# Kernel tuning notes

Measured on AMD Instinct MI355X. Metric: run time of the kernel, lower is better.

The kernel has to match this reference:

```python
import jax, jax.numpy as jnp
import numpy as np

N_NODES = 100000
N_EDGES = 1600000
D_IN = 64
D_H = 64


def setup_inputs() -> dict:
    key = jax.random.key(0)
    ks = jax.random.split(key, 8)
    inp = {
        "in_feat": jax.random.normal(ks[0], (N_NODES, D_IN), dtype=jnp.float32),
        "src": jax.random.randint(ks[1], (N_EDGES,), 0, N_NODES, dtype=jnp.int64)
        if jax.config.jax_enable_x64
        else jax.random.randint(ks[1], (N_EDGES,), 0, N_NODES).astype(jnp.int32),
        "dst": jax.random.randint(ks[2], (N_EDGES,), 0, N_NODES).astype(jnp.int32),
        "W_self1": jax.random.normal(ks[3], (D_H, D_IN), dtype=jnp.float32) * 0.1,
        "W_neigh1": jax.random.normal(ks[4], (D_H, D_IN), dtype=jnp.float32) * 0.1,
        "b1": jnp.zeros((D_H,), dtype=jnp.float32),
        "W_self2": jax.random.normal(ks[5], (D_H, D_H), dtype=jnp.float32) * 0.1,
        "W_neigh2": jax.random.normal(ks[6], (D_H, D_H), dtype=jnp.float32) * 0.1,
        "b2": jnp.zeros((D_H,), dtype=jnp.float32),
    }
    inp["src"] = inp["src"].astype(jnp.int32)
    return inp


def _sage_mean(x, src, dst, W_self, W_neigh, b, n_nodes):
    # mean aggregation over incoming edges: gather src feats, segment-sum at dst
    msg_sum = jax.ops.segment_sum(x[src], dst, num_segments=n_nodes)  # [N, D]
    deg = jax.ops.segment_sum(jnp.ones_like(dst, dtype=x.dtype), dst, num_segments=n_nodes)
    h_neigh = msg_sum / jnp.maximum(deg, 1.0)[:, None]
    # DGL SAGEConv: fc_self(h) + fc_neigh(h_neigh) + bias
    return x @ W_self.T + h_neigh @ W_neigh.T + b


def reference(in_feat, src, dst, W_self1, W_neigh1, b1, W_self2, W_neigh2, b2):
    n = in_feat.shape[0]
    h = _sage_mean(in_feat, src, dst, W_self1, W_neigh1, b1, n)
    # dropout in eval mode is identity; then relu
    h = jax.nn.relu(h)
    h = _sage_mean(h, src, dst, W_self2, W_neigh2, b2, n)
    return h
```

## Files before the change

### kernel.cpp

```cpp
#include <hip/hip_runtime.h>

#define NN 100000
#define NE 1600000
#define NROWS 100032
#define CAP 48
#define ZOFF (NN * 64)
#define NRANGE 12500
#define SCAT_GROUPS 8
#define SCAT_CHUNKS 196
#define SCAT_EPB 8192
#define SCAT_BLKS (SCAT_GROUPS * SCAT_CHUNKS)
#define CAST_BLKS 6250
#define WCAT_BLKS 64
#define ZCUR_BLKS 391
#define AGG_BLKS 3125

typedef __attribute__((ext_vector_type(8))) short short8;
typedef __attribute__((ext_vector_type(4))) float float4v;
typedef __attribute__((ext_vector_type(4))) int int4v;

__device__ inline unsigned short f2bf(float f)
{
    union { float f; unsigned u; } v; v.f = f;
    unsigned r = v.u + 0x7FFF + ((v.u >> 16) & 1);
    return (unsigned short)(r >> 16);
}
__device__ inline float bf2f(unsigned short h)
{
    union { unsigned u; float f; } v; v.u = ((unsigned)h) << 16; return v.f;
}

__global__ __launch_bounds__(256) void zero_kernel(int* __restrict__ cur)
{
    int i = blockIdx.x * 256 + threadIdx.x;
    if (i < NN) cur[i] = 0;
}

__global__ __launch_bounds__(256) void prep_kernel(
    const float* __restrict__ x,
    const float* __restrict__ Ws1, const float* __restrict__ Wn1,
    const float* __restrict__ Ws2, const float* __restrict__ Wn2,
    const int* __restrict__ src, const int* __restrict__ dst,
    unsigned short* __restrict__ XF, unsigned short* __restrict__ H1,
    unsigned short* __restrict__ W1, unsigned short* __restrict__ W2,
    int* __restrict__ cur, int* __restrict__ colb)
{
    const int b = blockIdx.x;
    const int tid = threadIdx.x;
    if (b < SCAT_BLKS) {
        const int g = b & 7;
        const int chunk = b >> 3;
        const int lo = g * NRANGE;
        const int hi = lo + NRANGE;
        const int base = chunk * SCAT_EPB;
        #pragma unroll
        for (int k = 0; k < 8; ++k) {
            int e = base + (k * 256 + tid) * 4;
            if (e < NE) {
                int4v s4 = __builtin_nontemporal_load((const int4v*)(src + e));
                int4v d4 = __builtin_nontemporal_load((const int4v*)(dst + e));
                int p;
                if (d4[0] >= lo && d4[0] < hi) {
                    p = atomicAdd(&cur[d4[0]], 1);
                    if (p < CAP) colb[(size_t)d4[0] * CAP + p] = s4[0] << 6;
                }
                if (d4[1] >= lo && d4[1] < hi) {
                    p = atomicAdd(&cur[d4[1]], 1);
                    if (p < CAP) colb[(size_t)d4[1] * CAP + p] = s4[1] << 6;
                }
                if (d4[2] >= lo && d4[2] < hi) {
                    p = atomicAdd(&cur[d4[2]], 1);
                    if (p < CAP) colb[(size_t)d4[2] * CAP + p] = s4[2] << 6;
                }
                if (d4[3] >= lo && d4[3] < hi) {
                    p = atomicAdd(&cur[d4[3]], 1);
                    if (p < CAP) colb[(size_t)d4[3] * CAP + p] = s4[3] << 6;
                }
            }
        }
    } else if (b < SCAT_BLKS + CAST_BLKS) {
        int t = (b - SCAT_BLKS) * 256 + tid;
        int n = t >> 4;
        int k4 = (t & 15) * 4;
        float4v v = __builtin_nontemporal_load(
            (const float4v*)(x + (size_t)n * 64 + k4));
        ushort4 o;
        o.x = f2bf(v[0]); o.y = f2bf(v[1]); o.z = f2bf(v[2]); o.w = f2bf(v[3]);
        *(ushort4*)(XF + (size_t)n * 64 + k4) = o;
    } else if (b < SCAT_BLKS + CAST_BLKS + WCAT_BLKS) {
        int id = (b - SCAT_BLKS - CAST_BLKS) * 256 + tid;
        int l = id >> 13;
        int r = id & 8191;
        int o = r >> 7, k = r & 127;
        const float* Ws = l ? Ws2 : Ws1;
        const float* Wn = l ? Wn2 : Wn1;
        float v = (k < 64) ? Ws[o * 64 + k] : Wn[o * 64 + (k - 64)];
        (l ? W2 : W1)[r] = f2bf(v);
    } else {
        if (tid < 32) {
            ushort4 z; z.x = 0; z.y = 0; z.z = 0; z.w = 0;
            unsigned short* base = (tid < 16) ? XF : H1;
            *(ushort4*)(base + (size_t)NN * 64 + (tid & 15) * 4) = z;
        }
    }
}

template <int LAYER1>
__global__ __launch_bounds__(256) void aggdense_kernel(
    const unsigned short* __restrict__ XIN,
    const int* __restrict__ cur,
    const int* __restrict__ colb,
    const unsigned short* __restrict__ Wcat,
    const float* __restrict__ bias,
    unsigned short* __restrict__ xout,
    float* __restrict__ fout)
{
    __shared__ __align__(16) unsigned short HN[32 * 72];
    const int tid = threadIdx.x;
    const int wave = tid >> 6;
    const int lane = tid & 63;
    const int g = lane >> 4;
    const int q = lane & 15;
    const int nbase = blockIdx.x * 32 + wave * 8;

    int cntv = (lane < 8) ? cur[nbase + lane] : 0;

    int cnt_nx = __shfl(cntv, 0, 64);
    int cc_nx = min(cnt_nx, CAP);
    int ci_nx = (lane < cc_nx) ? colb[(size_t)nbase * CAP + lane] : ZOFF;

    for (int i = 0; i < 8; ++i) {
        int n = nbase + i;
        int cnt = cnt_nx, cc = cc_nx, ci = ci_nx;
        if (i < 7) {
            cnt_nx = __shfl(cntv, i + 1, 64);
            cc_nx = min(cnt_nx, CAP);
            ci_nx = (lane < cc_nx) ? colb[(size_t)(n + 1) * CAP + lane] : ZOFF;
        }
        float a0 = 0.f, a1 = 0.f, a2 = 0.f, a3 = 0.f;
        for (int t = 0; t < cc; t += 16) {
            int i0 = __shfl(ci, t + g, 64);
            int i1 = __shfl(ci, t + 4 + g, 64);
            int i2 = __shfl(ci, t + 8 + g, 64);
            int i3 = __shfl(ci, t + 12 + g, 64);
            ushort4 v0 = *(const ushort4*)(XIN + i0 + q * 4);
            ushort4 v1 = *(const ushort4*)(XIN + i1 + q * 4);
            ushort4 v2 = *(const ushort4*)(XIN + i2 + q * 4);
            ushort4 v3 = *(const ushort4*)(XIN + i3 + q * 4);
            a0 += bf2f(v0.x) + bf2f(v1.x) + bf2f(v2.x) + bf2f(v3.x);
            a1 += bf2f(v0.y) + bf2f(v1.y) + bf2f(v2.y) + bf2f(v3.y);
            a2 += bf2f(v0.z) + bf2f(v1.z) + bf2f(v2.z) + bf2f(v3.z);
            a3 += bf2f(v0.w) + bf2f(v1.w) + bf2f(v2.w) + bf2f(v3.w);
        }
        a0 += __shfl_xor(a0, 16, 64); a0 += __shfl_xor(a0, 32, 64);
        a1 += __shfl_xor(a1, 16, 64); a1 += __shfl_xor(a1, 32, 64);
        a2 += __shfl_xor(a2, 16, 64); a2 += __shfl_xor(a2, 32, 64);
        a3 += __shfl_xor(a3, 16, 64); a3 += __shfl_xor(a3, 32, 64);
        float rdeg = 1.0f / fmaxf((float)cnt, 1.0f);
        if (g == 0) {
            ushort4 o;
            o.x = f2bf(a0 * rdeg); o.y = f2bf(a1 * rdeg);
            o.z = f2bf(a2 * rdeg); o.w = f2bf(a3 * rdeg);
            *(ushort4*)(&HN[(wave * 8 + i) * 72 + q * 4]) = o;
        }
    }
    __syncthreads();

    if (wave < 2) {
        const int mrow = lane & 15;
        const int kb = lane >> 4;
        const int row0 = blockIdx.x * 32 + wave * 16;

        short8 a[4];
        {
            const short* ax = (const short*)XIN + (size_t)(row0 + mrow) * 64 + kb * 8;
            const short* ah = (const short*)HN + (wave * 16 + mrow) * 72 + kb * 8;
            a[0] = *(const short8*)(ax);
            a[1] = *(const short8*)(ax + 32);
            a[2] = *(const short8*)(ah);
            a[3] = *(const short8*)(ah + 32);
        }

        float4v acc[4];
        #pragma unroll
        for (int c = 0; c < 4; ++c) acc[c] = (float4v){0.f, 0.f, 0.f, 0.f};

        #pragma unroll
        for (int c = 0; c < 4; ++c) {
            const short* brow = (const short*)Wcat + (c * 16 + mrow) * 128 + kb * 8;
            #pragma unroll
            for (int i = 0; i < 4; ++i) {
                short8 bfr = *(const short8*)(brow + i * 32);
                acc[c] = __builtin_amdgcn_mfma_f32_16x16x32_bf16(a[i], bfr, acc[c], 0, 0, 0);
            }
        }

        const int rbase = row0 + kb * 4;
        #pragma unroll
        for (int c = 0; c < 4; ++c) {
            int o = c * 16 + mrow;
            float bv = bias[o];
            #pragma unroll
            for (int r = 0; r < 4; ++r) {
                int node = rbase + r;
                float val = acc[c][r] + bv;
                if (LAYER1) {
                    xout[(size_t)node * 64 + o] = f2bf(fmaxf(val, 0.f));
                } else {
                    fout[(size_t)node * 64 + o] = val;
                }
            }
        }
    }
}

extern "C" void kernel_launch(void* const* d_in, const int* in_sizes, int n_in,
                              void* d_out, int out_size, void* d_ws, size_t ws_size,
                              hipStream_t stream)
{
    const float* in_feat = (const float*)d_in[0];
    const int*   src     = (const int*)d_in[1];
    const int*   dst     = (const int*)d_in[2];
    const float* Ws1     = (const float*)d_in[3];
    const float* Wn1     = (const float*)d_in[4];
    const float* b1      = (const float*)d_in[5];
    const float* Ws2     = (const float*)d_in[6];
    const float* Wn2     = (const float*)d_in[7];
    const float* b2      = (const float*)d_in[8];
    float* out = (float*)d_out;

    int* cur  = (int*)d_ws;
    int* colb = cur + NN;
    unsigned short* XF = (unsigned short*)(colb + (size_t)NN * CAP);
    unsigned short* H1 = XF + (size_t)NROWS * 64;
    unsigned short* W1 = H1 + (size_t)NROWS * 64;
    unsigned short* W2 = W1 + 8192;

    zero_kernel<<<ZCUR_BLKS, 256, 0, stream>>>(cur);

    prep_kernel<<<SCAT_BLKS + CAST_BLKS + WCAT_BLKS + 1, 256, 0, stream>>>(
        in_feat, Ws1, Wn1, Ws2, Wn2, src, dst, XF, H1, W1, W2, cur, colb);

    aggdense_kernel<1><<<AGG_BLKS, 256, 0, stream>>>(
        XF, cur, colb, W1, b1, H1, nullptr);

    aggdense_kernel<0><<<AGG_BLKS, 256, 0, stream>>>(
        H1, cur, colb, W2, b2, nullptr, out);
}
```

Baseline: 251.7 us.

## Split aggregation and dense into separate kernels with feature-sliced layout

Stores node features in four 16-column slices so each aggregation block gathers only a 32-byte slice per neighbor, which improves cache locality of the random gathers. The fused agg+dense kernel is split into a separate aggregation kernel (one node per 8 lanes, one slice per block) and a dense MFMA kernel that uses all four waves. Layer-1 output overwrites the input buffer in place. The cost is two extra kernel launches and a write and re-read of the aggregated features through global memory.

```diff
diff --git a/kernel.cpp b/kernel.cpp
--- a/kernel.cpp
+++ b/kernel.cpp
@@ -3,8 +3,9 @@
 #define NN 100000
 #define NE 1600000
 #define NROWS 100032
+#define SROW NROWS
 #define CAP 48
-#define ZOFF (NN * 64)
+#define DUMMY NN
 #define NRANGE 12500
 #define SCAT_GROUPS 8
 #define SCAT_CHUNKS 196
@@ -13,7 +14,9 @@
 #define CAST_BLKS 6250
 #define WCAT_BLKS 64
 #define ZCUR_BLKS 391
-#define AGG_BLKS 3125
+#define PAD_BLKS 2
+#define AGG_BLKS 12504
+#define DENSE_BLKS 1563
 
 typedef __attribute__((ext_vector_type(8))) short short8;
 typedef __attribute__((ext_vector_type(4))) float float4v;
@@ -41,7 +44,7 @@
     const float* __restrict__ Ws1, const float* __restrict__ Wn1,
     const float* __restrict__ Ws2, const float* __restrict__ Wn2,
     const int* __restrict__ src, const int* __restrict__ dst,
-    unsigned short* __restrict__ XF, unsigned short* __restrict__ H1,
+    unsigned short* __restrict__ XS, unsigned short* __restrict__ HNs,
     unsigned short* __restrict__ W1, unsigned short* __restrict__ W2,
     int* __restrict__ cur, int* __restrict__ colb)
 {
@@ -62,19 +65,19 @@
                 int p;
                 if (d4[0] >= lo && d4[0] < hi) {
                     p = atomicAdd(&cur[d4[0]], 1);
-                    if (p < CAP) colb[(size_t)d4[0] * CAP + p] = s4[0] << 6;
+                    if (p < CAP) colb[(size_t)d4[0] * CAP + p] = s4[0];
                 }
                 if (d4[1] >= lo && d4[1] < hi) {
                     p = atomicAdd(&cur[d4[1]], 1);
-                    if (p < CAP) colb[(size_t)d4[1] * CAP + p] = s4[1] << 6;
+                    if (p < CAP) colb[(size_t)d4[1] * CAP + p] = s4[1];
                 }
                 if (d4[2] >= lo && d4[2] < hi) {
                     p = atomicAdd(&cur[d4[2]], 1);
-                    if (p < CAP) colb[(size_t)d4[2] * CAP + p] = s4[2] << 6;
+                    if (p < CAP) colb[(size_t)d4[2] * CAP + p] = s4[2];
                 }
                 if (d4[3] >= lo && d4[3] < hi) {
                     p = atomicAdd(&cur[d4[3]], 1);
-                    if (p < CAP) colb[(size_t)d4[3] * CAP + p] = s4[3] << 6;
+                    if (p < CAP) colb[(size_t)d4[3] * CAP + p] = s4[3];
                 }
             }
         }
@@ -86,7 +89,7 @@
             (const float4v*)(x + (size_t)n * 64 + k4));
         ushort4 o;
         o.x = f2bf(v[0]); o.y = f2bf(v[1]); o.z = f2bf(v[2]); o.w = f2bf(v[3]);
-        *(ushort4*)(XF + (size_t)n * 64 + k4) = o;
+        *(ushort4*)(XS + ((size_t)(k4 >> 4) * SROW + n) * 16 + (k4 & 15)) = o;
     } else if (b < SCAT_BLKS + CAST_BLKS + WCAT_BLKS) {
         int id = (b - SCAT_BLKS - CAST_BLKS) * 256 + tid;
         int l = id >> 13;
@@ -97,118 +100,149 @@
         float v = (k < 64) ? Ws[o * 64 + k] : Wn[o * 64 + (k - 64)];
         (l ? W2 : W1)[r] = f2bf(v);
     } else {
-        if (tid < 32) {
+        unsigned short* base = (b == SCAT_BLKS + CAST_BLKS + WCAT_BLKS) ? XS : HNs;
+        for (int i = tid; i < 512; i += 256) {
+            int f = i >> 7;
+            int r = (i >> 2) & 31;
+            int q = i & 3;
             ushort4 z; z.x = 0; z.y = 0; z.z = 0; z.w = 0;
-            unsigned short* base = (tid < 16) ? XF : H1;
-            *(ushort4*)(base + (size_t)NN * 64 + (tid & 15) * 4) = z;
-        }
-    }
-}
-
-template <int LAYER1>
-__global__ __launch_bounds__(256) void aggdense_kernel(
-    const unsigned short* __restrict__ XIN,
+            *(ushort4*)(base + ((size_t)f * SROW + NN + r) * 16 + q * 4) = z;
+        }
+    }
+}
+
+__global__ __launch_bounds__(256) void agg_kernel(
+    const unsigned short* __restrict__ XS,
     const int* __restrict__ cur,
     const int* __restrict__ colb,
-    const unsigned short* __restrict__ Wcat,
-    const float* __restrict__ bias,
-    unsigned short* __restrict__ xout,
-    float* __restrict__ fout)
-{
-    __shared__ __align__(16) unsigned short HN[32 * 72];
+    unsigned short* __restrict__ HNs)
+{
+    const int b = blockIdx.x;
+    const int f = (b & 7) >> 1;
+    const int chunk = ((b >> 3) << 1) | (b & 1);
+    if (chunk >= NN / 32) return;
     const int tid = threadIdx.x;
     const int wave = tid >> 6;
     const int lane = tid & 63;
-    const int g = lane >> 4;
-    const int q = lane & 15;
-    const int nbase = blockIdx.x * 32 + wave * 8;
-
-    int cntv = (lane < 8) ? cur[nbase + lane] : 0;
-
-    int cnt_nx = __shfl(cntv, 0, 64);
-    int cc_nx = min(cnt_nx, CAP);
-    int ci_nx = (lane < cc_nx) ? colb[(size_t)nbase * CAP + lane] : ZOFF;
-
-    for (int i = 0; i < 8; ++i) {
-        int n = nbase + i;
-        int cnt = cnt_nx, cc = cc_nx, ci = ci_nx;
-        if (i < 7) {
-            cnt_nx = __shfl(cntv, i + 1, 64);
-            cc_nx = min(cnt_nx, CAP);
-            ci_nx = (lane < cc_nx) ? colb[(size_t)(n + 1) * CAP + lane] : ZOFF;
-        }
-        float a0 = 0.f, a1 = 0.f, a2 = 0.f, a3 = 0.f;
-        for (int t = 0; t < cc; t += 16) {
-            int i0 = __shfl(ci, t + g, 64);
-            int i1 = __shfl(ci, t + 4 + g, 64);
-            int i2 = __shfl(ci, t + 8 + g, 64);
-            int i3 = __shfl(ci, t + 12 + g, 64);
-            ushort4 v0 = *(const ushort4*)(XIN + i0 + q * 4);
-            ushort4 v1 = *(const ushort4*)(XIN + i1 + q * 4);
-            ushort4 v2 = *(const ushort4*)(XIN + i2 + q * 4);
-            ushort4 v3 = *(const ushort4*)(XIN + i3 + q * 4);
-            a0 += bf2f(v0.x) + bf2f(v1.x) + bf2f(v2.x) + bf2f(v3.x);
-            a1 += bf2f(v0.y) + bf2f(v1.y) + bf2f(v2.y) + bf2f(v3.y);
-            a2 += bf2f(v0.z) + bf2f(v1.z) + bf2f(v2.z) + bf2f(v3.z);
-            a3 += bf2f(v0.w) + bf2f(v1.w) + bf2f(v2.w) + bf2f(v3.w);
-        }
-        a0 += __shfl_xor(a0, 16, 64); a0 += __shfl_xor(a0, 32, 64);
-        a1 += __shfl_xor(a1, 16, 64); a1 += __shfl_xor(a1, 32, 64);
-        a2 += __shfl_xor(a2, 16, 64); a2 += __shfl_xor(a2, 32, 64);
-        a3 += __shfl_xor(a3, 16, 64); a3 += __shfl_xor(a3, 32, 64);
-        float rdeg = 1.0f / fmaxf((float)cnt, 1.0f);
-        if (g == 0) {
-            ushort4 o;
-            o.x = f2bf(a0 * rdeg); o.y = f2bf(a1 * rdeg);
-            o.z = f2bf(a2 * rdeg); o.w = f2bf(a3 * rdeg);
-            *(ushort4*)(&HN[(wave * 8 + i) * 72 + q * 4]) = o;
-        }
-    }
-    __syncthreads();
-
-    if (wave < 2) {
-        const int mrow = lane & 15;
-        const int kb = lane >> 4;
-        const int row0 = blockIdx.x * 32 + wave * 16;
-
-        short8 a[4];
-        {
-            const short* ax = (const short*)XIN + (size_t)(row0 + mrow) * 64 + kb * 8;
-            const short* ah = (const short*)HN + (wave * 16 + mrow) * 72 + kb * 8;
-            a[0] = *(const short8*)(ax);
-            a[1] = *(const short8*)(ax + 32);
-            a[2] = *(const short8*)(ah);
-            a[3] = *(const short8*)(ah + 32);
-        }
-
-        float4v acc[4];
-        #pragma unroll
-        for (int c = 0; c < 4; ++c) acc[c] = (float4v){0.f, 0.f, 0.f, 0.f};
-
-        #pragma unroll
-        for (int c = 0; c < 4; ++c) {
-            const short* brow = (const short*)Wcat + (c * 16 + mrow) * 128 + kb * 8;
+    const int j = lane >> 3;
+    const int s = lane & 7;
+    const int n = chunk * 32 + wave * 8 + j;
+    const int deg = cur[n];
+    const int cc = min(deg, CAP);
+    const int* lst = colb + (size_t)n * CAP;
+    const unsigned short* Xf = XS + (size_t)f * SROW * 16;
+
+    float acc0[8], acc1[8];
+    #pragma unroll
+    for (int k = 0; k < 8; ++k) { acc0[k] = 0.f; acc1[k] = 0.f; }
+
+    int si[4];
+    #pragma unroll
+    for (int r = 0; r < 4; ++r) {
+        int slot = s + r * 8;
+        si[r] = (slot < cc) ? __builtin_nontemporal_load(lst + slot) : DUMMY;
+    }
+    #pragma unroll
+    for (int r = 0; r < 4; ++r) {
+        const short8* p = (const short8*)(Xf + (size_t)si[r] * 16);
+        short8 v0 = p[0];
+        short8 v1 = p[1];
+        #pragma unroll
+        for (int k = 0; k < 8; ++k) {
+            acc0[k] += bf2f((unsigned short)v0[k]);
+            acc1[k] += bf2f((unsigned short)v1[k]);
+        }
+    }
+    if (__any(cc > 32)) {
+        #pragma unroll
+        for (int r = 4; r < 6; ++r) {
+            int slot = s + r * 8;
+            int sx = (slot < cc) ? __builtin_nontemporal_load(lst + slot) : DUMMY;
+            const short8* p = (const short8*)(Xf + (size_t)sx * 16);
+            short8 v0 = p[0];
+            short8 v1 = p[1];
             #pragma unroll
-            for (int i = 0; i < 4; ++i) {
-                short8 bfr = *(const short8*)(brow + i * 32);
-                acc[c] = __builtin_amdgcn_mfma_f32_16x16x32_bf16(a[i], bfr, acc[c], 0, 0, 0);
+            for (int k = 0; k < 8; ++k) {
+                acc0[k] += bf2f((unsigned short)v0[k]);
+                acc1[k] += bf2f((unsigned short)v1[k]);
             }
         }
-
-        const int rbase = row0 + kb * 4;
-        #pragma unroll
-        for (int c = 0; c < 4; ++c) {
-            int o = c * 16 + mrow;
-            float bv = bias[o];
-            #pragma unroll
-            for (int r = 0; r < 4; ++r) {
-                int node = rbase + r;
-                float val = acc[c][r] + bv;
-                if (LAYER1) {
-                    xout[(size_t)node * 64 + o] = f2bf(fmaxf(val, 0.f));
-                } else {
-                    fout[(size_t)node * 64 + o] = val;
-                }
+    }
+    #pragma unroll
+    for (int m = 1; m < 8; m <<= 1) {
+        #pragma unroll
+        for (int k = 0; k < 8; ++k) {
+            acc0[k] += __shfl_xor(acc0[k], m, 64);
+            acc1[k] += __shfl_xor(acc1[k], m, 64);
+        }
+    }
+    float rdeg = 1.0f / fmaxf((float)deg, 1.0f);
+    if (s < 2) {
+        short8 o;
+        #pragma unroll
+        for (int k = 0; k < 8; ++k) {
+            float v = (s == 0) ? acc0[k] : acc1[k];
+            o[k] = (short)f2bf(v * rdeg);
+        }
+        __builtin_nontemporal_store(o,
+            (short8*)(HNs + ((size_t)f * SROW + n) * 16 + s * 8));
+    }
+}
+
+template <int LAYER1>
+__global__ __launch_bounds__(256) void dense_kernel(
+    const unsigned short* XS,
+    const unsigned short* __restrict__ HNs,
+    const unsigned short* __restrict__ Wcat,
+    const float* __restrict__ bias,
+    unsigned short* xouts,
+    float* __restrict__ fout)
+{
+    const int tid = threadIdx.x;
+    const int wave = tid >> 6;
+    const int lane = tid & 63;
+    const int mrow = lane & 15;
+    const int kb = lane >> 4;
+    const int row0 = blockIdx.x * 64 + wave * 16;
+    const int n = row0 + mrow;
+
+    const int fs = kb >> 1;
+    const int off = (kb & 1) * 8;
+    short8 a[4];
+    a[0] = *(const short8*)(XS  + ((size_t)fs * SROW + n) * 16 + off);
+    a[1] = *(const short8*)(XS  + ((size_t)(2 + fs) * SROW + n) * 16 + off);
+    a[2] = *(const short8*)(HNs + ((size_t)fs * SROW + n) * 16 + off);
+    a[3] = *(const short8*)(HNs + ((size_t)(2 + fs) * SROW + n) * 16 + off);
+
+    float4v acc[4];
+    #pragma unroll
+    for (int c = 0; c < 4; ++c) acc[c] = (float4v){0.f, 0.f, 0.f, 0.f};
+
+    #pragma unroll
+    for (int c = 0; c < 4; ++c) {
+        const short* brow = (const short*)Wcat + (c * 16 + mrow) * 128 + kb * 8;
+        #pragma unroll
+        for (int i = 0; i < 4; ++i) {
+            short8 bfr = *(const short8*)(brow + i * 32);
+            acc[c] = __builtin_amdgcn_mfma_f32_16x16x32_bf16(a[i], bfr, acc[c], 0, 0, 0);
+        }
+    }
+
+    const int rbase = row0 + kb * 4;
+    #pragma unroll
+    for (int c = 0; c < 4; ++c) {
+        int o = c * 16 + mrow;
+        float bv = bias[o];
+        #pragma unroll
+        for (int r = 0; r < 4; ++r) {
+            int node = rbase + r;
+            float val = acc[c][r] + bv;
+            if (LAYER1) {
+                if (node < NN)
+                    xouts[((size_t)c * SROW + node) * 16 + mrow] =
+                        f2bf(fmaxf(val, 0.f));
+            } else {
+                if (node < NN) fout[(size_t)node * 64 + o] = val;
             }
         }
     }
@@ -231,19 +265,23 @@
 
     int* cur  = (int*)d_ws;
     int* colb = cur + NN;
-    unsigned short* XF = (unsigned short*)(colb + (size_t)NN * CAP);
-    unsigned short* H1 = XF + (size_t)NROWS * 64;
-    unsigned short* W1 = H1 + (size_t)NROWS * 64;
-    unsigned short* W2 = W1 + 8192;
+    unsigned short* XS  = (unsigned short*)(colb + (size_t)NN * CAP);
+    unsigned short* HNs = XS + (size_t)4 * SROW * 16;
+    unsigned short* W1  = HNs + (size_t)4 * SROW * 16;
+    unsigned short* W2  = W1 + 8192;
 
     zero_kernel<<<ZCUR_BLKS, 256, 0, stream>>>(cur);
 
-    prep_kernel<<<SCAT_BLKS + CAST_BLKS + WCAT_BLKS + 1, 256, 0, stream>>>(
-        in_feat, Ws1, Wn1, Ws2, Wn2, src, dst, XF, H1, W1, W2, cur, colb);
-
-    aggdense_kernel<1><<<AGG_BLKS, 256, 0, stream>>>(
-        XF, cur, colb, W1, b1, H1, nullptr);
-
-    aggdense_kernel<0><<<AGG_BLKS, 256, 0, stream>>>(
-        H1, cur, colb, W2, b2, nullptr, out);
-}
+    prep_kernel<<<SCAT_BLKS + CAST_BLKS + WCAT_BLKS + PAD_BLKS, 256, 0, stream>>>(
+        in_feat, Ws1, Wn1, Ws2, Wn2, src, dst, XS, HNs, W1, W2, cur, colb);
+
+    agg_kernel<<<AGG_BLKS, 256, 0, stream>>>(XS, cur, colb, HNs);
+
+    dense_kernel<1><<<DENSE_BLKS, 256, 0, stream>>>(
+        XS, HNs, W1, b1, XS, nullptr);
+
+    agg_kernel<<<AGG_BLKS, 256, 0, stream>>>(XS, cur, colb, HNs);
+
+    dense_kernel<0><<<DENSE_BLKS, 256, 0, stream>>>(
+        XS, HNs, W2, b2, nullptr, out);
+}
```

Result: slower. 352.3 us (+40.0%).
